# Performance work log

Hardware: AMD Instinct MI355X
Metric: run time of the kernel (lower is better)

Reference implementation:

```python
import jax, jax.numpy as jnp
import numpy as np

EMB = 512
HEADS = 8
B, T = 4, 1024


def setup_inputs() -> dict:
    key = jax.random.key(0)
    k1, k2, k3, k4, k5 = jax.random.split(key, 5)
    scale = 1.0 / np.sqrt(EMB)
    x = jax.random.normal(k1, (B, T, EMB), dtype=jnp.float32)
    # Linear(emb, emb*heads, bias=False) weights, stored as [in, out] for x @ W
    Wk = jax.random.normal(k2, (EMB, EMB * HEADS), dtype=jnp.float32) * scale
    Wq = jax.random.normal(k3, (EMB, EMB * HEADS), dtype=jnp.float32) * scale
    Wv = jax.random.normal(k4, (EMB, EMB * HEADS), dtype=jnp.float32) * scale
    Wu = jax.random.normal(k5, (EMB * HEADS, EMB), dtype=jnp.float32) * (1.0 / np.sqrt(EMB * HEADS))
    return {"x": x, "Wk": Wk, "Wq": Wq, "Wv": Wv, "Wu": Wu}


def reference(x, Wk, Wq, Wv, Wu):
    b, t, k = x.shape
    h = HEADS
    # projections -> [b, h, t, k]
    keys = (x @ Wk).reshape(b, t, h, k).transpose(0, 2, 1, 3)
    queries = (x @ Wq).reshape(b, t, h, k).transpose(0, 2, 1, 3)
    values = (x @ Wv).reshape(b, t, h, k).transpose(0, 2, 1, 3)
    # NOTE: original computes bmm(keys, queries^T): dot[i,j] = key_i . query_j
    dot = jnp.einsum('bhik,bhjk->bhij', keys, queries)  # [b,h,t,t]
    # mask_fn: only upper-triangle (offset=1) entries that are EXACTLY zero get -inf
    triu = jnp.triu(jnp.ones((t, t), dtype=bool), k=1)
    final_mask = triu & (dot == 0)
    dot = jnp.where(final_mask, -jnp.inf, dot)
    attn = jax.nn.softmax(dot, axis=-1)
    out = jnp.einsum('bhij,bhjk->bhik', attn, values)  # [b,h,t,k]
    out = out.transpose(0, 2, 1, 3).reshape(b, t, h * k)
    return out @ Wu
```

## Files before the change

### kernel.cpp

```cpp
#include <hip/hip_runtime.h>
#include <stdint.h>

typedef _Float16 f16x8 __attribute__((ext_vector_type(8)));
typedef float f32x4 __attribute__((ext_vector_type(4)));

__device__ __forceinline__ unsigned short f2h(float f) {
  _Float16 h = (_Float16)f;
  return __builtin_bit_cast(unsigned short, h);
}

#if __has_builtin(__builtin_amdgcn_global_load_lds)
#define HAVE_GLL 1
__device__ __forceinline__ void gload_lds16(const void* g, void* l) {
  auto gp = reinterpret_cast<const __attribute__((address_space(1))) void*>(
      reinterpret_cast<uintptr_t>(g));
  auto lp = reinterpret_cast<__attribute__((address_space(3))) void*>(
      reinterpret_cast<uintptr_t>(l));
  __builtin_amdgcn_global_load_lds(gp, lp, 16, 0, 0);
}
#else
#define HAVE_GLL 0
#endif

__device__ __forceinline__ void transpose_core(const float* in, unsigned short* out,
                                               int R, int C, int c0, int r0) {
  __shared__ float t[32][33];
  int tx = threadIdx.x & 31, ty = threadIdx.x >> 5;
#pragma unroll
  for (int i = 0; i < 32; i += 8)
    t[ty + i][tx] = in[(long)(r0 + ty + i) * C + (c0 + tx)];
  __syncthreads();
#pragma unroll
  for (int i = 0; i < 32; i += 8)
    out[(long)(c0 + ty + i) * R + (r0 + tx)] = f2h(t[tx][ty + i]);
}

__global__ __launch_bounds__(256) void k_setup(
    const float* __restrict__ x, const float* __restrict__ Wq, const float* __restrict__ Wk,
    const float* __restrict__ Wv, const float* __restrict__ Wu,
    unsigned short* __restrict__ Xh, unsigned short* __restrict__ Wqt,
    unsigned short* __restrict__ Wkt, unsigned short* __restrict__ Wvh,
    unsigned short* __restrict__ Wut) {
  int z = blockIdx.z;
  if (z == 0) {
    transpose_core(Wq, Wqt, 512, 4096, blockIdx.x * 32, blockIdx.y * 32);
  } else if (z == 1) {
    transpose_core(Wk, Wkt, 512, 4096, blockIdx.x * 32, blockIdx.y * 32);
  } else if (z == 2) {
    transpose_core(Wu, Wut, 4096, 512, blockIdx.y * 32, blockIdx.x * 32);
  } else {
    const float* in = (z == 3) ? x : Wv;
    unsigned short* out = (z == 3) ? Xh : Wvh;
    int i = (blockIdx.y * 128 + blockIdx.x) * 256 + threadIdx.x;
    float4 v = reinterpret_cast<const float4*>(in)[i];
    ushort4 o;
    o.x = f2h(v.x); o.y = f2h(v.y); o.z = f2h(v.z); o.w = f2h(v.w);
    reinterpret_cast<ushort4*>(out)[i] = o;
  }
}

template <int OUT>
__device__ __forceinline__ void gemm_core(unsigned short* __restrict__ As,
                                          unsigned short* __restrict__ Bs,
                                          const unsigned short* __restrict__ A,
                                          const unsigned short* __restrict__ B,
                                          void* __restrict__ Cv, int K, int lda, int ldb,
                                          int ldc, long coff, int m0, int n0) {
  int tid = threadIdx.x;
  int wid = tid >> 6, lane = tid & 63;
  int wm = (wid >> 1) * 64, wn = (wid & 1) * 64;
  int rq = lane >> 4, rl = lane & 15;

  f32x4 acc[4][4];
#pragma unroll
  for (int i = 0; i < 4; ++i)
#pragma unroll
    for (int j = 0; j < 4; ++j) acc[i][j] = (f32x4){0.f, 0.f, 0.f, 0.f};

#if HAVE_GLL
  int cg = (lane & 7) ^ ((lane >> 3) & 7);
  int rl8 = lane >> 3;
#endif

  for (int k0 = 0; k0 < K; k0 += 64) {
    __syncthreads();
#if HAVE_GLL
#pragma unroll
    for (int t = 0; t < 4; ++t) {
      int r = wid * 32 + t * 8;
      gload_lds16(&A[(long)(m0 + r + rl8) * lda + k0 + cg * 8], &As[r * 64]);
      gload_lds16(&B[(long)(n0 + r + rl8) * ldb + k0 + cg * 8], &Bs[r * 64]);
    }
#else
#pragma unroll
    for (int it = 0; it < 4; ++it) {
      int idx = tid + it * 256;
      int r = idx >> 3, c = idx & 7;
      int cs = c ^ (r & 7);
      *reinterpret_cast<uint4*>(&As[r * 64 + cs * 8]) =
          *reinterpret_cast<const uint4*>(&A[(long)(m0 + r) * lda + k0 + c * 8]);
      *reinterpret_cast<uint4*>(&Bs[r * 64 + cs * 8]) =
          *reinterpret_cast<const uint4*>(&B[(long)(n0 + r) * ldb + k0 + c * 8]);
    }
#endif
    __syncthreads();
#pragma unroll
    for (int ks = 0; ks < 2; ++ks) {
      f16x8 af[4], bfr[4];
      int kc = ks * 4 + rq;
#pragma unroll
      for (int i = 0; i < 4; ++i) {
        int ra = wm + i * 16 + rl;
        af[i] = *reinterpret_cast<const f16x8*>(&As[ra * 64 + ((kc ^ (ra & 7)) << 3)]);
        int rb = wn + i * 16 + rl;
        bfr[i] = *reinterpret_cast<const f16x8*>(&Bs[rb * 64 + ((kc ^ (rb & 7)) << 3)]);
      }
#pragma unroll
      for (int i = 0; i < 4; ++i)
#pragma unroll
        for (int j = 0; j < 4; ++j)
          acc[i][j] = __builtin_amdgcn_mfma_f32_16x16x32_f16(af[i], bfr[j], acc[i][j], 0, 0, 0);
    }
  }

#pragma unroll
  for (int i = 0; i < 4; ++i)
#pragma unroll
    for (int j = 0; j < 4; ++j)
#pragma unroll
      for (int r = 0; r < 4; ++r) {
        int row = m0 + wm + i * 16 + rq * 4 + r;
        int col = n0 + wn + j * 16 + rl;
        float v = acc[i][j][r];
        if (OUT == 1)
          reinterpret_cast<unsigned short*>(Cv)[coff + (long)row * ldc + col] = f2h(v);
        else if (OUT == 0)
          reinterpret_cast<float*>(Cv)[coff + (long)row * ldc + col] = v;
        else if (OUT == 2)
          atomicAdd(&reinterpret_cast<float*>(Cv)[coff + (long)row * ldc + col], v);
        else {
          long addr = (long)(col >> 10) * 4194304 + (long)(row & 511) * 8192 +
                      ((row >> 9) << 10) + (col & 1023);
          reinterpret_cast<unsigned short*>(Cv)[addr] = f2h(v);
        }
      }
}

#define DECL_LDS \
  __shared__ unsigned short As[128 * 64]; \
  __shared__ unsigned short Bs[128 * 64];

template <int OUT>
__global__ __launch_bounds__(256, 2) void k_gemm_btx(
    const unsigned short* __restrict__ A, const unsigned short* __restrict__ B,
    void* __restrict__ Cv, int K, int lda, int ldb, int ldc,
    long oAo, long oAi, long oBo, long oBi, long oCo, long oCi, int zdiv,
    int sx, int sy) {
  DECL_LDS
  int c = blockIdx.x, w = blockIdx.y;
  int z = c + 8 * (w >> (sx + sy));
  int y = (w >> sx) & ((1 << sy) - 1);
  int x = w & ((1 << sx) - 1);
  A += (long)(z / zdiv) * oAo + (long)(z % zdiv) * oAi;
  B += (long)(z / zdiv) * oBo + (long)(z % zdiv) * oBi;
  long coff = (long)(z / zdiv) * oCo + (long)(z % zdiv) * oCi;
  gemm_core<OUT>(As, Bs, A, B, Cv, K, lda, ldb, ldc, coff, y * 128, x * 128);
}

__global__ __launch_bounds__(256, 2) void k_gemm_qkv(
    const unsigned short* __restrict__ X, const unsigned short* __restrict__ Wqt,
    const unsigned short* __restrict__ Wkt, const unsigned short* __restrict__ Wvut,
    unsigned short* __restrict__ Qb, unsigned short* __restrict__ Kb,
    unsigned short* __restrict__ VUb) {
  DECL_LDS
  int c = blockIdx.x, w = blockIdx.y;
  int z = w >> 7;
  int r = w & 127;
  if (z < 2) {
    int x = 4 * c + (r & 3), y = r >> 2;
    gemm_core<1>(As, Bs, X, (z == 0) ? Wqt : Wkt, (z == 0) ? Qb : Kb, 512, 512, 512,
                 4096, 0, y * 128, x * 128);
  } else {
    int y = 4 * c + (r & 3), x = r >> 2;
    gemm_core<3>(As, Bs, Wvut, X, VUb, 512, 512, 512, 0, 0, y * 128, x * 128);
  }
}

__global__ __launch_bounds__(256, 2) void k_gemm_out(
    const unsigned short* __restrict__ Pb, const unsigned short* __restrict__ VUb,
    float* __restrict__ out) {
  DECL_LDS
  int c = blockIdx.x, w = blockIdx.y;
  int g = c + 8 * (w >> 4);
  int r = w & 15;
  int b = g >> 3, kc = (g >> 1) & 3, ih = g & 1;
  int y = ih * 4 + (r >> 2);
  int x = r & 3;
  gemm_core<2>(As, Bs, Pb + (long)b * 8388608 + kc * 2048,
               VUb + (long)b * 4194304 + kc * 2048, out, 2048, 8192, 8192, 512,
               (long)b * 524288, y * 128, x * 128);
}

__global__ __launch_bounds__(256) void k_softmax_x(unsigned short* __restrict__ S) {
  int g = blockIdx.y * 4 + (threadIdx.x >> 6);
  int b = g >> 10, i = g & 1023;
  long base = (long)b * 8388608 + (long)i * 8192 + (long)blockIdx.x * 1024;
  int lane = threadIdx.x & 63;
  f16x8* p = reinterpret_cast<f16x8*>(S + base);
  f16x8 a = p[lane * 2], bb = p[lane * 2 + 1];
  float v[16];
#pragma unroll
  for (int q = 0; q < 8; ++q) { v[q] = (float)a[q]; v[8 + q] = (float)bb[q]; }
  float m = v[0];
#pragma unroll
  for (int q = 1; q < 16; ++q) m = fmaxf(m, v[q]);
#pragma unroll
  for (int o = 32; o; o >>= 1) m = fmaxf(m, __shfl_xor(m, o));
  float s = 0.f;
#pragma unroll
  for (int q = 0; q < 16; ++q) { v[q] = __expf(v[q] - m); s += v[q]; }
#pragma unroll
  for (int o = 32; o; o >>= 1) s += __shfl_xor(s, o);
  float inv = 1.0f / s;
  f16x8 oa, ob;
#pragma unroll
  for (int q = 0; q < 8; ++q) {
    oa[q] = (_Float16)(v[q] * inv);
    ob[q] = (_Float16)(v[8 + q] * inv);
  }
  p[lane * 2] = oa;
  p[lane * 2 + 1] = ob;
}

__global__ void k_sentinel(float* out, float v) { out[0] = v; }

extern "C" void kernel_launch(void* const* d_in, const int* in_sizes, int n_in,
                              void* d_out, int out_size, void* d_ws, size_t ws_size,
                              hipStream_t stream) {
  const float* x  = (const float*)d_in[0];
  const float* Wk = (const float*)d_in[1];
  const float* Wq = (const float*)d_in[2];
  const float* Wv = (const float*)d_in[3];
  const float* Wu = (const float*)d_in[4];
  float* out = (float*)d_out;

  const long SZ_X = 4096L * 512;
  const long SZ_W = 512L * 4096;
  const size_t NEED = 188743680;

  if (ws_size < NEED) {
    hipMemsetAsync(d_out, 0, (size_t)out_size * 4, stream);
    k_sentinel<<<1, 1, 0, stream>>>(out, (float)ws_size);
    return;
  }

  char* p = (char*)d_ws;
  unsigned short* Xbf  = (unsigned short*)p; p += SZ_X * 2;
  unsigned short* Wqt  = (unsigned short*)p; p += SZ_W * 2;
  unsigned short* Wkt  = (unsigned short*)p; p += SZ_W * 2;
  unsigned short* Wut  = (unsigned short*)p; p += SZ_W * 2;
  unsigned short* Wvut = (unsigned short*)p; p += SZ_W * 2;
  unsigned short* Qb   = (unsigned short*)p; p += 4096L * 4096 * 2;
  unsigned short* Kb   = (unsigned short*)p; p += 4096L * 4096 * 2;
  unsigned short* Pb   = (unsigned short*)p; p += 4096L * 8192 * 2;
  unsigned short* VUb  = (unsigned short*)p;
  unsigned short* Wvh  = VUb;

  hipMemsetAsync(d_out, 0, (size_t)out_size * 4, stream);

  k_setup<<<dim3(128, 16, 5), 256, 0, stream>>>(x, Wq, Wk, Wv, Wu, Xbf, Wqt, Wkt, Wvh, Wut);

  k_gemm_btx<1><<<dim3(8, 16), 256, 0, stream>>>(
      Wut, Wvh, Wvut, 512, 4096, 4096, 512,
      512, 0, 512, 0, 262144, 0, 1, 2, 2);

  k_gemm_qkv<<<dim3(8, 384), 256, 0, stream>>>(Xbf, Wqt, Wkt, Wvut, Qb, Kb, VUb);

  k_gemm_btx<1><<<dim3(8, 256), 256, 0, stream>>>(
      Kb, Qb, Pb, 512, 4096, 4096, 8192,
      4194304, 512, 4194304, 512, 8388608, 1024, 8, 3, 3);

  k_softmax_x<<<dim3(8, 1024), 256, 0, stream>>>(Pb);

  k_gemm_out<<<dim3(8, 64), 256, 0, stream>>>(Pb, VUb, out);
}
```

Measured before the change: 283.4 us.

## Merge independent GEMM launches into fewer grids and reuse VU in natural layout

```diff
diff --git a/kernel.cpp b/kernel.cpp
--- a/kernel.cpp
+++ b/kernel.cpp
@@ -59,13 +59,13 @@
   }
 }
 
-template <int OUT>
+template <int OUT, int BVU>
 __device__ __forceinline__ void gemm_core(unsigned short* __restrict__ As,
                                           unsigned short* __restrict__ Bs,
                                           const unsigned short* __restrict__ A,
                                           const unsigned short* __restrict__ B,
                                           void* __restrict__ Cv, int K, int lda, int ldb,
-                                          int ldc, long coff, int m0, int n0) {
+                                          int ldc, long coff, int m0, int n0, int kbase) {
   int tid = threadIdx.x;
   int wid = tid >> 6, lane = tid & 63;
   int wm = (wid >> 1) * 64, wn = (wid & 1) * 64;
@@ -83,13 +83,20 @@
 #endif
 
   for (int k0 = 0; k0 < K; k0 += 64) {
+    long bko;
+    if (BVU) {
+      int kk = kbase + k0;
+      bko = (long)(kk >> 10) * 2097152 + (kk & 1023);
+    } else {
+      bko = k0;
+    }
     __syncthreads();
 #if HAVE_GLL
 #pragma unroll
     for (int t = 0; t < 4; ++t) {
       int r = wid * 32 + t * 8;
       gload_lds16(&A[(long)(m0 + r + rl8) * lda + k0 + cg * 8], &As[r * 64]);
-      gload_lds16(&B[(long)(n0 + r + rl8) * ldb + k0 + cg * 8], &Bs[r * 64]);
+      gload_lds16(&B[(long)(n0 + r + rl8) * ldb + bko + cg * 8], &Bs[r * 64]);
     }
 #else
 #pragma unroll
@@ -100,7 +107,7 @@
       *reinterpret_cast<uint4*>(&As[r * 64 + cs * 8]) =
           *reinterpret_cast<const uint4*>(&A[(long)(m0 + r) * lda + k0 + c * 8]);
       *reinterpret_cast<uint4*>(&Bs[r * 64 + cs * 8]) =
-          *reinterpret_cast<const uint4*>(&B[(long)(n0 + r) * ldb + k0 + c * 8]);
+          *reinterpret_cast<const uint4*>(&B[(long)(n0 + r) * ldb + bko + c * 8]);
     }
 #endif
     __syncthreads();
@@ -134,15 +141,8 @@
         float v = acc[i][j][r];
         if (OUT == 1)
           reinterpret_cast<unsigned short*>(Cv)[coff + (long)row * ldc + col] = f2h(v);
-        else if (OUT == 0)
-          reinterpret_cast<float*>(Cv)[coff + (long)row * ldc + col] = v;
-        else if (OUT == 2)
+        else
           atomicAdd(&reinterpret_cast<float*>(Cv)[coff + (long)row * ldc + col], v);
-        else {
-          long addr = (long)(col >> 10) * 4194304 + (long)(row & 511) * 8192 +
-                      ((row >> 9) << 10) + (col & 1023);
-          reinterpret_cast<unsigned short*>(Cv)[addr] = f2h(v);
-        }
       }
 }
 
@@ -150,44 +150,60 @@
   __shared__ unsigned short As[128 * 64]; \
   __shared__ unsigned short Bs[128 * 64];
 
-template <int OUT>
-__global__ __launch_bounds__(256, 2) void k_gemm_btx(
-    const unsigned short* __restrict__ A, const unsigned short* __restrict__ B,
-    void* __restrict__ Cv, int K, int lda, int ldb, int ldc,
-    long oAo, long oAi, long oBo, long oBi, long oCo, long oCi, int zdiv,
-    int sx, int sy) {
+__global__ __launch_bounds__(256, 2) void k_gemm_qkw(
+    const unsigned short* __restrict__ X, const unsigned short* __restrict__ Wqt,
+    const unsigned short* __restrict__ Wkt, const unsigned short* __restrict__ Wvh,
+    const unsigned short* __restrict__ Wut, unsigned short* __restrict__ Qb,
+    unsigned short* __restrict__ Kb, unsigned short* __restrict__ Wvut) {
   DECL_LDS
   int c = blockIdx.x, w = blockIdx.y;
-  int z = c + 8 * (w >> (sx + sy));
-  int y = (w >> sx) & ((1 << sy) - 1);
-  int x = w & ((1 << sx) - 1);
-  A += (long)(z / zdiv) * oAo + (long)(z % zdiv) * oAi;
-  B += (long)(z / zdiv) * oBo + (long)(z % zdiv) * oBi;
-  long coff = (long)(z / zdiv) * oCo + (long)(z % zdiv) * oCi;
-  gemm_core<OUT>(As, Bs, A, B, Cv, K, lda, ldb, ldc, coff, y * 128, x * 128);
-}
-
-__global__ __launch_bounds__(256, 2) void k_gemm_qkv(
-    const unsigned short* __restrict__ X, const unsigned short* __restrict__ Wqt,
-    const unsigned short* __restrict__ Wkt, const unsigned short* __restrict__ Wvut,
-    unsigned short* __restrict__ Qb, unsigned short* __restrict__ Kb,
-    unsigned short* __restrict__ VUb) {
+  const unsigned short *A, *B;
+  unsigned short* C;
+  int lda, ldb, ldc, m0, n0;
+  long coff;
+  if (w < 256) {
+    int z = w >> 7, r = w & 127;
+    int x = 4 * c + (r & 3), y = r >> 2;
+    A = X; B = (z == 0) ? Wqt : Wkt; C = (z == 0) ? Qb : Kb;
+    lda = 512; ldb = 512; ldc = 4096; coff = 0; m0 = y * 128; n0 = x * 128;
+  } else {
+    int wp = w - 256;
+    A = Wut + c * 512; B = Wvh + c * 512; C = Wvut + (long)c * 262144;
+    lda = 4096; ldb = 4096; ldc = 512; coff = 0;
+    m0 = ((wp >> 2) & 3) * 128; n0 = (wp & 3) * 128;
+  }
+  gemm_core<1, 0>(As, Bs, A, B, C, 512, lda, ldb, ldc, coff, m0, n0, 0);
+}
+
+__global__ __launch_bounds__(256, 2) void k_gemm_sv(
+    const unsigned short* __restrict__ X, const unsigned short* __restrict__ Qb,
+    const unsigned short* __restrict__ Kb, const unsigned short* __restrict__ Wvut,
+    unsigned short* __restrict__ Pb, unsigned short* __restrict__ VUt) {
   DECL_LDS
   int c = blockIdx.x, w = blockIdx.y;
-  int z = w >> 7;
-  int r = w & 127;
-  if (z < 2) {
-    int x = 4 * c + (r & 3), y = r >> 2;
-    gemm_core<1>(As, Bs, X, (z == 0) ? Wqt : Wkt, (z == 0) ? Qb : Kb, 512, 512, 512,
-                 4096, 0, y * 128, x * 128);
+  const unsigned short *A, *B;
+  unsigned short* C;
+  int lda, ldb, ldc, m0, n0;
+  long coff;
+  if (w < 256) {
+    int z = c + 8 * (w >> 6), t = w & 63;
+    int b = z >> 3, h = z & 7;
+    long off = (long)b * 4194304 + h * 512;
+    A = Kb + off; B = Qb + off; C = Pb;
+    lda = 4096; ldb = 4096; ldc = 8192;
+    coff = (long)b * 8388608 + h * 1024;
+    m0 = (t >> 3) * 128; n0 = (t & 7) * 128;
   } else {
-    int y = 4 * c + (r & 3), x = r >> 2;
-    gemm_core<3>(As, Bs, Wvut, X, VUb, 512, 512, 512, 0, 0, y * 128, x * 128);
-  }
+    int wp = w - 256;
+    A = Wvut; B = X; C = VUt;
+    lda = 512; ldb = 512; ldc = 4096; coff = 0;
+    m0 = (4 * c + (wp & 3)) * 128; n0 = (wp >> 2) * 128;
+  }
+  gemm_core<1, 0>(As, Bs, A, B, C, 512, lda, ldb, ldc, coff, m0, n0, 0);
 }
 
 __global__ __launch_bounds__(256, 2) void k_gemm_out(
-    const unsigned short* __restrict__ Pb, const unsigned short* __restrict__ VUb,
+    const unsigned short* __restrict__ Pb, const unsigned short* __restrict__ VUt,
     float* __restrict__ out) {
   DECL_LDS
   int c = blockIdx.x, w = blockIdx.y;
@@ -196,9 +212,9 @@
   int b = g >> 3, kc = (g >> 1) & 3, ih = g & 1;
   int y = ih * 4 + (r >> 2);
   int x = r & 3;
-  gemm_core<2>(As, Bs, Pb + (long)b * 8388608 + kc * 2048,
-               VUb + (long)b * 4194304 + kc * 2048, out, 2048, 8192, 8192, 512,
-               (long)b * 524288, y * 128, x * 128);
+  gemm_core<2, 1>(As, Bs, Pb + (long)b * 8388608 + kc * 2048, VUt + (long)b * 1024,
+                  out, 2048, 8192, 4096, 512, (long)b * 524288, y * 128, x * 128,
+                  kc * 2048);
 }
 
 __global__ __launch_bounds__(256) void k_softmax_x(unsigned short* __restrict__ S) {
@@ -263,24 +279,18 @@
   unsigned short* Qb   = (unsigned short*)p; p += 4096L * 4096 * 2;
   unsigned short* Kb   = (unsigned short*)p; p += 4096L * 4096 * 2;
   unsigned short* Pb   = (unsigned short*)p; p += 4096L * 8192 * 2;
-  unsigned short* VUb  = (unsigned short*)p;
-  unsigned short* Wvh  = VUb;
+  unsigned short* VUt  = (unsigned short*)p;
+  unsigned short* Wvh  = VUt;
 
   hipMemsetAsync(d_out, 0, (size_t)out_size * 4, stream);
 
   k_setup<<<dim3(128, 16, 5), 256, 0, stream>>>(x, Wq, Wk, Wv, Wu, Xbf, Wqt, Wkt, Wvh, Wut);
 
-  k_gemm_btx<1><<<dim3(8, 16), 256, 0, stream>>>(
-      Wut, Wvh, Wvut, 512, 4096, 4096, 512,
-      512, 0, 512, 0, 262144, 0, 1, 2, 2);
-
-  k_gemm_qkv<<<dim3(8, 384), 256, 0, stream>>>(Xbf, Wqt, Wkt, Wvut, Qb, Kb, VUb);
-
-  k_gemm_btx<1><<<dim3(8, 256), 256, 0, stream>>>(
-      Kb, Qb, Pb, 512, 4096, 4096, 8192,
-      4194304, 512, 4194304, 512, 8388608, 1024, 8, 3, 3);
+  k_gemm_qkw<<<dim3(8, 272), 256, 0, stream>>>(Xbf, Wqt, Wkt, Wvh, Wut, Qb, Kb, Wvut);
+
+  k_gemm_sv<<<dim3(8, 384), 256, 0, stream>>>(Xbf, Qb, Kb, Wvut, Pb, VUt);
 
   k_softmax_x<<<dim3(8, 1024), 256, 0, stream>>>(Pb);
 
-  k_gemm_out<<<dim3(8, 64), 256, 0, stream>>>(Pb, VUb, out);
-}
+  k_gemm_out<<<dim3(8, 64), 256, 0, stream>>>(Pb, VUt, out);
+}
```

New measurement: 283.4 us. Within noise of the previous version (+0.0%).
